# Kernel tuning notes

Measured on AMD Instinct MI355X. Metric: run time of the kernel, lower is better.

The kernel has to match this reference:

```python
import math
import jax, jax.numpy as jnp
import numpy as np

DN = ('NCHW', 'OIHW', 'NCHW')

def _conv2d(x, w, b, stride, padding='VALID'):
    y = jax.lax.conv_general_dilated(x, w, window_strides=stride, padding=padding,
                                     dimension_numbers=DN)
    return y + b[None, :, None, None]

def _same_padding_conv(x, w, b, s):
    # replicate torch same_padding_conv: ceil-mode SAME padding, then VALID conv
    H, W = x.shape[2], x.shape[3]
    kh, kw = w.shape[2], w.shape[3]
    out_h, out_w = math.ceil(H / s[0]), math.ceil(W / s[1])
    pad_h = max((out_h - 1) * s[0] + kh - H, 0)
    pad_w = max((out_w - 1) * s[1] + kw - W, 0)
    pt, pl = pad_h // 2, pad_w // 2
    x = jnp.pad(x, ((0, 0), (0, 0), (pt, pad_h - pt), (pl, pad_w - pl)))
    return _conv2d(x, w, b, s)

def _leaky(x):
    return jax.nn.leaky_relu(x, negative_slope=0.2)

def setup_inputs() -> dict:
    key = jax.random.key(0)
    ks = jax.random.split(key, 8)
    B, cin, cout, H, W = 2, 16, 24, 384, 1280
    fl = jax.random.normal(ks[0], (B, cin, H, W), jnp.float32)
    fr = jax.random.normal(ks[1], (B, cin, H, W), jnp.float32)
    w_em = jax.random.normal(ks[2], (cout, cin, 4, 4), jnp.float32) * 0.05
    b_em = jax.random.normal(ks[3], (cout,), jnp.float32) * 0.05
    w_rc = jax.random.normal(ks[4], (cout, cout, 1, 1), jnp.float32) * 0.1
    b_rc = jax.random.normal(ks[5], (cout,), jnp.float32) * 0.05
    w_tf = jax.random.normal(ks[6], (13, cout + 1, 1, 1), jnp.float32) * 0.1
    b_tf = jax.random.normal(ks[7], (13,), jnp.float32) * 0.05
    return {'feature_left': fl, 'feature_right': fr, 'max_disp': 64,
            'w_em': w_em, 'b_em': b_em, 'w_rc': w_rc, 'b_rc': b_rc,
            'w_tf': w_tf, 'b_tf': b_tf}

def reference(feature_left, feature_right, max_disp, w_em, b_em, w_rc, b_rc, w_tf, b_tf):
    # left branch: 4x4 conv, stride (4,4), VALID (torch default padding=0)
    fl = _leaky(_conv2d(_leaky(_conv2d(feature_left, w_em, b_em, (4, 4))), w_rc, b_rc, (1, 1)))
    # right branch: same-padding conv with stride (4,1) -> full width retained
    fr = _leaky(_conv2d(_leaky(_same_padding_conv(feature_right, w_em, b_em, (4, 1))), w_rc, b_rc, (1, 1)))
    B, C, Hq, Wq = fl.shape
    Wr = fr.shape[3]
    # clipped gather indices: idx[d, x] = clip(4*x - d + 1, 0, Wr-1)
    d = jnp.arange(max_disp)[:, None]          # [D,1]
    x = jnp.arange(Wq)[None, :]                # [1,Wq]
    idx = jnp.clip(4 * x - d + 1, 0, Wr - 1)   # [D,Wq]
    fr_g = jnp.take(fr, idx, axis=3)           # [B,C,H,D,Wq]
    # L1 cost over channels -> [B,D,H,Wq]
    cost_volume = jnp.sum(jnp.abs(fl[:, :, :, None, :] - fr_g), axis=1).transpose(0, 2, 1, 3)
    cost_f = jnp.min(cost_volume, axis=1, keepdims=True)                  # [B,1,H,Wq]
    d_init = jnp.argmin(cost_volume, axis=1, keepdims=True).astype(fl.dtype)
    p_init = jnp.concatenate([cost_f, fl], axis=1)
    p_init = _leaky(_conv2d(p_init, w_tf, b_tf, (1, 1)))                  # [B,13,H,Wq]
    z = jnp.zeros_like(d_init)
    out = jnp.concatenate([d_init, z, z, p_init], axis=1)                 # [B,16,H,Wq]
    return out, cost_volume
```

## Files before the change

kernel.cpp:

```cpp
#include <hip/hip_runtime.h>

#define B_   2
#define CIN  16
#define HIN  384
#define WIN  1280
#define CO   24
#define HQ   96
#define WL   320
#define WR   1280
#define DMAX 64

__device__ __forceinline__ float lk(float v) { return v >= 0.f ? v : 0.2f * v; }

__global__ __launch_bounds__(256) void k_left(
    const float* __restrict__ x, const float* __restrict__ w_em,
    const float* __restrict__ b_em, const float* __restrict__ w_rc,
    const float* __restrict__ b_rc, float* __restrict__ out)
{
    __shared__ float smem[CO * CIN * 16];
    __shared__ float swt[CO * CO];
    __shared__ float sbe[CO], sbr[CO];

    for (int i = threadIdx.x; i < CO * CIN * 16; i += 256) smem[i] = w_em[i];
    for (int i = threadIdx.x; i < CO * CO; i += 256) swt[i] = w_rc[(i % CO) * CO + (i / CO)];
    if (threadIdx.x < CO) { sbe[threadIdx.x] = b_em[threadIdx.x]; sbr[threadIdx.x] = b_rc[threadIdx.x]; }
    __syncthreads();

    const int t = threadIdx.x;
    const int half = t >> 7, pxl = t & 127;
    const int obase = half * 12;
    const int flat = blockIdx.x * 128 + pxl;
    const int j = flat % WL, h = (flat / WL) % HQ, b = flat / (WL * HQ);

    float acc[12];
#pragma unroll
    for (int oo = 0; oo < 12; ++oo) acc[oo] = sbe[obase + oo];

    for (int c = 0; c < CIN; ++c) {
#pragma unroll
        for (int kh = 0; kh < 4; ++kh) {
            const float4 v = *(const float4*)(x + ((size_t)(b * CIN + c) * HIN + 4 * h + kh) * WIN + 4 * j);
#pragma unroll
            for (int oo = 0; oo < 12; ++oo) {
                const float4 wv = *(const float4*)&smem[(((obase + oo) * CIN + c) * 4 + kh) * 4];
                acc[oo] += v.x * wv.x + v.y * wv.y + v.z * wv.z + v.w * wv.w;
            }
        }
    }
    __syncthreads();
#pragma unroll
    for (int oo = 0; oo < 12; ++oo) smem[(obase + oo) * 128 + pxl] = lk(acc[oo]);
    __syncthreads();

    float acc2[12];
#pragma unroll
    for (int oo = 0; oo < 12; ++oo) acc2[oo] = sbr[obase + oo];
    for (int c = 0; c < CO; ++c) {
        const float in_c = smem[c * 128 + pxl];
#pragma unroll
        for (int oo = 0; oo < 12; ++oo) acc2[oo] += in_c * swt[c * CO + obase + oo];
    }
#pragma unroll
    for (int oo = 0; oo < 12; ++oo)
        out[((size_t)(b * CO + obase + oo) * HQ + h) * WL + j] = lk(acc2[oo]);
}

__global__ __launch_bounds__(256) void k_right(
    const float* __restrict__ x, const float* __restrict__ w_em,
    const float* __restrict__ b_em, const float* __restrict__ w_rc,
    const float* __restrict__ b_rc, float* __restrict__ out)
{
    __shared__ __align__(16) float sw[CO * CIN * 16];
    __shared__ float swt[CO * CO];
    __shared__ float sbe[CO], sbr[CO];

    for (int i = threadIdx.x; i < CO * CIN * 16; i += 256) sw[i] = w_em[i];
    for (int i = threadIdx.x; i < CO * CO; i += 256) swt[i] = w_rc[(i % CO) * CO + (i / CO)];
    if (threadIdx.x < CO) { sbe[threadIdx.x] = b_em[threadIdx.x]; sbr[threadIdx.x] = b_rc[threadIdx.x]; }
    __syncthreads();

    const int t = threadIdx.x;
    const int L = t & 63, quarter = t >> 6;
    const int obase = quarter * 6;
    const int row = blockIdx.x / 5, jbase = (blockIdx.x % 5) * 256;
    const int b = row / HQ, h = row % HQ;

    const bool vm1 = (jbase + 4 * L) > 0;
    const bool vp  = (jbase + 4 * L + 4) < WIN;
    const int  om1 = vm1 ? (4 * L - 2) : 0;
    const int  op4 = vp  ? (4 * L + 4) : 0;

    float acc[4][6];
#pragma unroll
    for (int k = 0; k < 4; ++k)
#pragma unroll
        for (int oo = 0; oo < 6; ++oo) acc[k][oo] = sbe[obase + oo];

    for (int c = 0; c < CIN; ++c) {
#pragma unroll
        for (int kh = 0; kh < 4; ++kh) {
            const float* xr = x + ((size_t)(b * CIN + c) * HIN + 4 * h + kh) * WIN + jbase;
            const float4  v = *(const float4*)(xr + 4 * L);
            const float2  A = *(const float2*)(xr + om1);
            const float2  C = *(const float2*)(xr + op4);
            float in[7];
            in[0] = vm1 ? A.y : 0.f;
            in[1] = v.x; in[2] = v.y; in[3] = v.z; in[4] = v.w;
            in[5] = vp ? C.x : 0.f;
            in[6] = vp ? C.y : 0.f;
#pragma unroll
            for (int oo = 0; oo < 6; ++oo) {
                const float4 wv = *(const float4*)&sw[(((obase + oo) * CIN + c) * 4 + kh) * 4];
#pragma unroll
                for (int k = 0; k < 4; ++k)
                    acc[k][oo] += in[k] * wv.x + in[k + 1] * wv.y + in[k + 2] * wv.z + in[k + 3] * wv.w;
            }
        }
    }
    __syncthreads();
#pragma unroll
    for (int oo = 0; oo < 6; ++oo) {
        float4 st = make_float4(lk(acc[0][oo]), lk(acc[1][oo]), lk(acc[2][oo]), lk(acc[3][oo]));
        *(float4*)&sw[(obase + oo) * 256 + 4 * L] = st;
    }
    __syncthreads();

    float acc2[CO];
#pragma unroll
    for (int o = 0; o < CO; ++o) acc2[o] = sbr[o];
    for (int c = 0; c < CO; ++c) {
        const float in_c = sw[c * 256 + t];
#pragma unroll
        for (int o = 0; o < CO; ++o) acc2[o] += in_c * swt[c * CO + o];
    }
#pragma unroll
    for (int o = 0; o < CO; ++o)
        out[((size_t)(b * CO + o) * HQ + h) * WR + jbase + t] = lk(acc2[o]);
}

__global__ __launch_bounds__(256) void k_cost(
    const float* __restrict__ fl, const float* __restrict__ fr,
    const float* __restrict__ wtf, const float* __restrict__ btf,
    float* __restrict__ out, float* __restrict__ cost)
{
    __shared__ float frs[CO * 324];
    __shared__ float sbest[256];
    __shared__ int   sbd[256];

    const int t  = threadIdx.x;
    const int j  = t & 63;
    const int w  = t >> 6;
    const int jc = blockIdx.x % 5;
    const int r  = blockIdx.x / 5;
    const int h  = r % HQ, b = r / HQ;
    const int j0 = jc * 64;
    const int jg = j0 + j;
    const int colbase = 4 * j0 - 64;

    for (int idx = t; idx < CO * 320; idx += 256) {
        const int c = idx / 320, Wd = idx % 320;
        const int col = colbase + Wd;
        frs[c * 324 + 2 + Wd] = fr[((size_t)(b * CO + c) * HQ + h) * WR + (col > 0 ? col : 0)];
    }
    __syncthreads();

    float acc[4][4];
#pragma unroll
    for (int q = 0; q < 4; ++q)
#pragma unroll
        for (int rr = 0; rr < 4; ++rr) acc[q][rr] = 0.f;

    for (int c = 0; c < CO; ++c) {
        const float flc = fl[((size_t)(b * CO + c) * HQ + h) * WL + jg];
        const float* base = &frs[c * 324 + 4 * j + 64];
#pragma unroll
        for (int q = 0; q < 4; ++q) {
            const int D = 4 * w + q;
            const float4 v = *(const float4*)(base - 4 * D);
            acc[q][0] += fabsf(flc - v.w);
            acc[q][1] += fabsf(flc - v.z);
            acc[q][2] += fabsf(flc - v.y);
            acc[q][3] += fabsf(flc - v.x);
        }
    }

#pragma unroll
    for (int q = 0; q < 4; ++q)
#pragma unroll
        for (int rr = 0; rr < 4; ++rr) {
            const int d = 16 * w + 4 * q + rr;
            cost[((size_t)(b * DMAX + d) * HQ + h) * WL + jg] = acc[q][rr];
        }

    float best = acc[0][0]; int bd = 16 * w;
#pragma unroll
    for (int q = 0; q < 4; ++q)
#pragma unroll
        for (int rr = 0; rr < 4; ++rr) {
            if (q == 0 && rr == 0) continue;
            const int d = 16 * w + 4 * q + rr;
            if (acc[q][rr] < best) { best = acc[q][rr]; bd = d; }
        }
    sbest[t] = best; sbd[t] = bd;
    __syncthreads();

    if (t < 64) {
        float cur = sbest[j]; int curd = sbd[j];
#pragma unroll
        for (int g = 1; g < 4; ++g) {
            const float v = sbest[g * 64 + j];
            if (v < cur) { cur = v; curd = sbd[g * 64 + j]; }
        }
        float flr[CO];
#pragma unroll
        for (int c = 0; c < CO; ++c) flr[c] = fl[((size_t)(b * CO + c) * HQ + h) * WL + jg];
#pragma unroll
        for (int o = 0; o < 13; ++o) {
            float a = btf[o] + wtf[o * 25] * cur;
#pragma unroll
            for (int c = 0; c < CO; ++c) a += wtf[o * 25 + 1 + c] * flr[c];
            out[((size_t)(b * 16 + 3 + o) * HQ + h) * WL + jg] = lk(a);
        }
        out[((size_t)(b * 16 + 0) * HQ + h) * WL + jg] = (float)curd;
        out[((size_t)(b * 16 + 1) * HQ + h) * WL + jg] = 0.f;
        out[((size_t)(b * 16 + 2) * HQ + h) * WL + jg] = 0.f;
    }
}

extern "C" void kernel_launch(void* const* d_in, const int* in_sizes, int n_in,
                              void* d_out, int out_size, void* d_ws, size_t ws_size,
                              hipStream_t stream) {
    const float* fl_in = (const float*)d_in[0];
    const float* fr_in = (const float*)d_in[1];
    const float* w_em = (const float*)d_in[3];
    const float* b_em = (const float*)d_in[4];
    const float* w_rc = (const float*)d_in[5];
    const float* b_rc = (const float*)d_in[6];
    const float* w_tf = (const float*)d_in[7];
    const float* b_tf = (const float*)d_in[8];

    float* out  = (float*)d_out;
    float* cost = out + (size_t)B_ * 16 * HQ * WL;

    float* fl_ws = (float*)d_ws;
    float* fr_ws = fl_ws + (size_t)B_ * CO * HQ * WL;

    hipLaunchKernelGGL(k_right, dim3(960), dim3(256), 0, stream,
                       fr_in, w_em, b_em, w_rc, b_rc, fr_ws);
    hipLaunchKernelGGL(k_left,  dim3(480), dim3(256), 0, stream,
                       fl_in, w_em, b_em, w_rc, b_rc, fl_ws);
    hipLaunchKernelGGL(k_cost,  dim3(960), dim3(256), 0, stream,
                       fl_ws, fr_ws, w_tf, b_tf, out, cost);
}
```

Before: 248.6 us.

## Merge left/right embedding kernels into one launch with double-buffered input loads

The separate left and right embedding kernels become a single kernel of 1440 blocks. Every third block does left-branch work and the rest do right-branch work, so both branches share the GPU at once and one launch is removed. The input channel loop is software-pipelined with two register buffers, so global loads for the next channel are in flight while the current one is computed. This raises register pressure and may lower occupancy. The interleaved branch blocks can also diverge in runtime.

```diff
diff --git a/kernel.cpp b/kernel.cpp
--- a/kernel.cpp
+++ b/kernel.cpp
@@ -12,63 +12,64 @@
 
 __device__ __forceinline__ float lk(float v) { return v >= 0.f ? v : 0.2f * v; }
 
-__global__ __launch_bounds__(256) void k_left(
-    const float* __restrict__ x, const float* __restrict__ w_em,
-    const float* __restrict__ b_em, const float* __restrict__ w_rc,
-    const float* __restrict__ b_rc, float* __restrict__ out)
-{
-    __shared__ float smem[CO * CIN * 16];
-    __shared__ float swt[CO * CO];
-    __shared__ float sbe[CO], sbr[CO];
-
-    for (int i = threadIdx.x; i < CO * CIN * 16; i += 256) smem[i] = w_em[i];
-    for (int i = threadIdx.x; i < CO * CO; i += 256) swt[i] = w_rc[(i % CO) * CO + (i / CO)];
-    if (threadIdx.x < CO) { sbe[threadIdx.x] = b_em[threadIdx.x]; sbr[threadIdx.x] = b_rc[threadIdx.x]; }
-    __syncthreads();
-
-    const int t = threadIdx.x;
-    const int half = t >> 7, pxl = t & 127;
-    const int obase = half * 12;
-    const int flat = blockIdx.x * 128 + pxl;
-    const int j = flat % WL, h = (flat / WL) % HQ, b = flat / (WL * HQ);
-
-    float acc[12];
-#pragma unroll
-    for (int oo = 0; oo < 12; ++oo) acc[oo] = sbe[obase + oo];
-
-    for (int c = 0; c < CIN; ++c) {
-#pragma unroll
-        for (int kh = 0; kh < 4; ++kh) {
-            const float4 v = *(const float4*)(x + ((size_t)(b * CIN + c) * HIN + 4 * h + kh) * WIN + 4 * j);
-#pragma unroll
-            for (int oo = 0; oo < 12; ++oo) {
-                const float4 wv = *(const float4*)&smem[(((obase + oo) * CIN + c) * 4 + kh) * 4];
-                acc[oo] += v.x * wv.x + v.y * wv.y + v.z * wv.z + v.w * wv.w;
-            }
-        }
-    }
-    __syncthreads();
-#pragma unroll
-    for (int oo = 0; oo < 12; ++oo) smem[(obase + oo) * 128 + pxl] = lk(acc[oo]);
-    __syncthreads();
-
-    float acc2[12];
-#pragma unroll
-    for (int oo = 0; oo < 12; ++oo) acc2[oo] = sbr[obase + oo];
-    for (int c = 0; c < CO; ++c) {
-        const float in_c = smem[c * 128 + pxl];
-#pragma unroll
-        for (int oo = 0; oo < 12; ++oo) acc2[oo] += in_c * swt[c * CO + obase + oo];
-    }
-#pragma unroll
-    for (int oo = 0; oo < 12; ++oo)
-        out[((size_t)(b * CO + obase + oo) * HQ + h) * WL + j] = lk(acc2[oo]);
-}
-
-__global__ __launch_bounds__(256) void k_right(
-    const float* __restrict__ x, const float* __restrict__ w_em,
-    const float* __restrict__ b_em, const float* __restrict__ w_rc,
-    const float* __restrict__ b_rc, float* __restrict__ out)
+struct RBuf { float4 v[4]; float2 A[4]; float2 C[4]; };
+struct LBuf { float4 v[4]; };
+
+__device__ __forceinline__ void r_issue(RBuf& B, const float* xrow,
+                                        int L4, int om1, int op4) {
+#pragma unroll
+    for (int kh = 0; kh < 4; ++kh) {
+        const float* p = xrow + kh * WIN;
+        B.v[kh] = *(const float4*)(p + L4);
+        B.A[kh] = *(const float2*)(p + om1);
+        B.C[kh] = *(const float2*)(p + op4);
+    }
+}
+
+__device__ __forceinline__ void r_comp(const RBuf& B, float (&acc)[4][6],
+                                       const float* sw, int obase, int c,
+                                       bool vm1, bool vp) {
+#pragma unroll
+    for (int kh = 0; kh < 4; ++kh) {
+        float in[7];
+        in[0] = vm1 ? B.A[kh].y : 0.f;
+        in[1] = B.v[kh].x; in[2] = B.v[kh].y; in[3] = B.v[kh].z; in[4] = B.v[kh].w;
+        in[5] = vp ? B.C[kh].x : 0.f;
+        in[6] = vp ? B.C[kh].y : 0.f;
+#pragma unroll
+        for (int oo = 0; oo < 6; ++oo) {
+            const float4 wv = *(const float4*)&sw[(((obase + oo) * CIN + c) * 4 + kh) * 4];
+#pragma unroll
+            for (int k = 0; k < 4; ++k)
+                acc[k][oo] += in[k] * wv.x + in[k + 1] * wv.y + in[k + 2] * wv.z + in[k + 3] * wv.w;
+        }
+    }
+}
+
+__device__ __forceinline__ void l_issue(LBuf& B, const float* xrow) {
+#pragma unroll
+    for (int kh = 0; kh < 4; ++kh)
+        B.v[kh] = *(const float4*)(xrow + kh * WIN);
+}
+
+__device__ __forceinline__ void l_comp(const LBuf& B, float (&acc)[12],
+                                       const float* sw, int obase, int c) {
+#pragma unroll
+    for (int kh = 0; kh < 4; ++kh) {
+        const float4 v = B.v[kh];
+#pragma unroll
+        for (int oo = 0; oo < 12; ++oo) {
+            const float4 wv = *(const float4*)&sw[(((obase + oo) * CIN + c) * 4 + kh) * 4];
+            acc[oo] += v.x * wv.x + v.y * wv.y + v.z * wv.z + v.w * wv.w;
+        }
+    }
+}
+
+__global__ __launch_bounds__(256) void k_em(
+    const float* __restrict__ xl, const float* __restrict__ xr,
+    const float* __restrict__ w_em, const float* __restrict__ b_em,
+    const float* __restrict__ w_rc, const float* __restrict__ b_rc,
+    float* __restrict__ out_l, float* __restrict__ out_r)
 {
     __shared__ __align__(16) float sw[CO * CIN * 16];
     __shared__ float swt[CO * CO];
@@ -80,62 +81,100 @@
     __syncthreads();
 
     const int t = threadIdx.x;
-    const int L = t & 63, quarter = t >> 6;
-    const int obase = quarter * 6;
-    const int row = blockIdx.x / 5, jbase = (blockIdx.x % 5) * 256;
-    const int b = row / HQ, h = row % HQ;
-
-    const bool vm1 = (jbase + 4 * L) > 0;
-    const bool vp  = (jbase + 4 * L + 4) < WIN;
-    const int  om1 = vm1 ? (4 * L - 2) : 0;
-    const int  op4 = vp  ? (4 * L + 4) : 0;
-
-    float acc[4][6];
-#pragma unroll
-    for (int k = 0; k < 4; ++k)
-#pragma unroll
-        for (int oo = 0; oo < 6; ++oo) acc[k][oo] = sbe[obase + oo];
-
-    for (int c = 0; c < CIN; ++c) {
-#pragma unroll
-        for (int kh = 0; kh < 4; ++kh) {
-            const float* xr = x + ((size_t)(b * CIN + c) * HIN + 4 * h + kh) * WIN + jbase;
-            const float4  v = *(const float4*)(xr + 4 * L);
-            const float2  A = *(const float2*)(xr + om1);
-            const float2  C = *(const float2*)(xr + op4);
-            float in[7];
-            in[0] = vm1 ? A.y : 0.f;
-            in[1] = v.x; in[2] = v.y; in[3] = v.z; in[4] = v.w;
-            in[5] = vp ? C.x : 0.f;
-            in[6] = vp ? C.y : 0.f;
-#pragma unroll
-            for (int oo = 0; oo < 6; ++oo) {
-                const float4 wv = *(const float4*)&sw[(((obase + oo) * CIN + c) * 4 + kh) * 4];
-#pragma unroll
-                for (int k = 0; k < 4; ++k)
-                    acc[k][oo] += in[k] * wv.x + in[k + 1] * wv.y + in[k + 2] * wv.z + in[k + 3] * wv.w;
-            }
-        }
-    }
-    __syncthreads();
-#pragma unroll
-    for (int oo = 0; oo < 6; ++oo) {
-        float4 st = make_float4(lk(acc[0][oo]), lk(acc[1][oo]), lk(acc[2][oo]), lk(acc[3][oo]));
-        *(float4*)&sw[(obase + oo) * 256 + 4 * L] = st;
-    }
-    __syncthreads();
-
-    float acc2[CO];
-#pragma unroll
-    for (int o = 0; o < CO; ++o) acc2[o] = sbr[o];
-    for (int c = 0; c < CO; ++c) {
-        const float in_c = sw[c * 256 + t];
-#pragma unroll
-        for (int o = 0; o < CO; ++o) acc2[o] += in_c * swt[c * CO + o];
-    }
-#pragma unroll
-    for (int o = 0; o < CO; ++o)
-        out[((size_t)(b * CO + o) * HQ + h) * WR + jbase + t] = lk(acc2[o]);
+    const size_t cstride = (size_t)HIN * WIN;
+
+    if (blockIdx.x % 3 == 0) {
+        const int lb = blockIdx.x / 3;
+        const int half = t >> 7, pxl = t & 127;
+        const int obase = half * 12;
+        const int flat = lb * 128 + pxl;
+        const int j = flat % WL, h = (flat / WL) % HQ, b = flat / (WL * HQ);
+        const float* xc = xl + ((size_t)(b * CIN) * HIN + 4 * h) * WIN + 4 * j;
+
+        float acc[12];
+#pragma unroll
+        for (int oo = 0; oo < 12; ++oo) acc[oo] = sbe[obase + oo];
+
+        LBuf P, Q;
+        l_issue(P, xc);
+        for (int c = 0; c < CIN - 2; c += 2) {
+            l_issue(Q, xc + (c + 1) * cstride);
+            l_comp(P, acc, sw, obase, c);
+            l_issue(P, xc + (c + 2) * cstride);
+            l_comp(Q, acc, sw, obase, c + 1);
+        }
+        l_issue(Q, xc + (CIN - 1) * cstride);
+        l_comp(P, acc, sw, obase, CIN - 2);
+        l_comp(Q, acc, sw, obase, CIN - 1);
+
+        __syncthreads();
+#pragma unroll
+        for (int oo = 0; oo < 12; ++oo) sw[(obase + oo) * 128 + pxl] = lk(acc[oo]);
+        __syncthreads();
+
+        float acc2[12];
+#pragma unroll
+        for (int oo = 0; oo < 12; ++oo) acc2[oo] = sbr[obase + oo];
+        for (int c = 0; c < CO; ++c) {
+            const float in_c = sw[c * 128 + pxl];
+#pragma unroll
+            for (int oo = 0; oo < 12; ++oo) acc2[oo] += in_c * swt[c * CO + obase + oo];
+        }
+#pragma unroll
+        for (int oo = 0; oo < 12; ++oo)
+            out_l[((size_t)(b * CO + obase + oo) * HQ + h) * WL + j] = lk(acc2[oo]);
+    } else {
+        const int rb = blockIdx.x - blockIdx.x / 3 - 1;
+        const int L = t & 63, quarter = t >> 6;
+        const int obase = quarter * 6;
+        const int row = rb / 5, jbase = (rb % 5) * 256;
+        const int b = row / HQ, h = row % HQ;
+
+        const bool vm1 = (jbase + 4 * L) > 0;
+        const bool vp  = (jbase + 4 * L + 4) < WIN;
+        const int  om1 = vm1 ? (4 * L - 2) : 0;
+        const int  op4 = vp  ? (4 * L + 4) : 0;
+        const int  L4  = 4 * L;
+        const float* xc = xr + ((size_t)(b * CIN) * HIN + 4 * h) * WIN + jbase;
+
+        float acc[4][6];
+#pragma unroll
+        for (int k = 0; k < 4; ++k)
+#pragma unroll
+            for (int oo = 0; oo < 6; ++oo) acc[k][oo] = sbe[obase + oo];
+
+        RBuf P, Q;
+        r_issue(P, xc, L4, om1, op4);
+        for (int c = 0; c < CIN - 2; c += 2) {
+            r_issue(Q, xc + (c + 1) * cstride, L4, om1, op4);
+            r_comp(P, acc, sw, obase, c, vm1, vp);
+            r_issue(P, xc + (c + 2) * cstride, L4, om1, op4);
+            r_comp(Q, acc, sw, obase, c + 1, vm1, vp);
+        }
+        r_issue(Q, xc + (CIN - 1) * cstride, L4, om1, op4);
+        r_comp(P, acc, sw, obase, CIN - 2, vm1, vp);
+        r_comp(Q, acc, sw, obase, CIN - 1, vm1, vp);
+
+        __syncthreads();
+#pragma unroll
+        for (int oo = 0; oo < 6; ++oo) {
+            float4 st = make_float4(lk(acc[0][oo]), lk(acc[1][oo]), lk(acc[2][oo]), lk(acc[3][oo]));
+            *(float4*)&sw[(obase + oo) * 256 + 4 * L] = st;
+        }
+        __syncthreads();
+
+        float acc2[CO];
+#pragma unroll
+        for (int o = 0; o < CO; ++o) acc2[o] = sbr[o];
+        for (int c = 0; c < CO; ++c) {
+            const float in_c = sw[c * 256 + t];
+#pragma unroll
+            for (int o = 0; o < CO; ++o) acc2[o] += in_c * swt[c * CO + o];
+        }
+#pragma unroll
+        for (int o = 0; o < CO; ++o)
+            out_r[((size_t)(b * CO + o) * HQ + h) * WR + jbase + t] = lk(acc2[o]);
+    }
 }
 
 __global__ __launch_bounds__(256) void k_cost(
@@ -245,10 +284,8 @@
     float* fl_ws = (float*)d_ws;
     float* fr_ws = fl_ws + (size_t)B_ * CO * HQ * WL;
 
-    hipLaunchKernelGGL(k_right, dim3(960), dim3(256), 0, stream,
-                       fr_in, w_em, b_em, w_rc, b_rc, fr_ws);
-    hipLaunchKernelGGL(k_left,  dim3(480), dim3(256), 0, stream,
-                       fl_in, w_em, b_em, w_rc, b_rc, fl_ws);
-    hipLaunchKernelGGL(k_cost,  dim3(960), dim3(256), 0, stream,
+    hipLaunchKernelGGL(k_em, dim3(1440), dim3(256), 0, stream,
+                       fl_in, fr_in, w_em, b_em, w_rc, b_rc, fl_ws, fr_ws);
+    hipLaunchKernelGGL(k_cost, dim3(960), dim3(256), 0, stream,
                        fl_ws, fr_ws, w_tf, b_tf, out, cost);
 }
```

Result: slower. 281.0 us (+13.0%).
